# Optimization experiments

Measured on AMD Instinct MI355X. Metric: run time of the kernel, lower is better.

The kernel has to match this reference:

```python
import jax, jax.numpy as jnp
import numpy as np

DIM = 512
HIDDEN = 2048
BATCH = 16384
NUM_VECTORS = 3


def _mlp(z, W1, b1, W2, b2, W3, b3):
    # 3-layer tanh MLP: dim -> hidden -> hidden -> dim
    h = jnp.tanh(z @ W1.T + b1)
    h = jnp.tanh(h @ W2.T + b2)
    return h @ W3.T + b3


def setup_inputs() -> dict:
    key = jax.random.key(0)
    ks = jax.random.split(key, 10)
    t = jnp.zeros((1,), dtype=jnp.float32)
    augmented_state = jax.random.normal(ks[0], (BATCH, DIM + 1), dtype=jnp.float32)
    epsilons = jax.random.normal(ks[1], (NUM_VECTORS, BATCH, DIM), dtype=jnp.float32)
    # Xavier-normal-ish init with gain 0.1 (final layer randomized instead of the
    # original zero-init so outputs/grads are non-trivial for kernel testing).
    def xavier(k, fan_out, fan_in, gain=0.1):
        std = gain * np.sqrt(2.0 / (fan_in + fan_out))
        return (jax.random.normal(k, (fan_out, fan_in), dtype=jnp.float32) * std)
    W1 = xavier(ks[2], HIDDEN, DIM)
    b1 = jnp.zeros((HIDDEN,), dtype=jnp.float32)
    W2 = xavier(ks[3], HIDDEN, HIDDEN)
    b2 = jnp.zeros((HIDDEN,), dtype=jnp.float32)
    W3 = xavier(ks[4], DIM, HIDDEN)
    b3 = jnp.zeros((DIM,), dtype=jnp.float32)
    return {"t": t, "augmented_state": augmented_state, "epsilons": epsilons,
            "W1": W1, "b1": b1, "W2": W2, "b2": b2, "W3": W3, "b3": b3}


def reference(t, augmented_state, epsilons, W1, b1, W2, b2, W3, b3):
    dim = W1.shape[1]
    z = augmented_state[:, :dim]                      # [B, dim]
    dz_dt = _mlp(z, W1, b1, W2, b2, W3, b3)           # [B, dim]
    # torch code computes g = d(sum f(z))/dz = J^T @ 1 (same for every loop
    # iteration since only epsilon is resampled), then averages (g * eps).sum(1).
    g = jax.grad(lambda zz: _mlp(zz, W1, b1, W2, b2, W3, b3).sum())(z)  # [B, dim]
    num_vectors = epsilons.shape[0]
    trace = jnp.einsum('kbd,bd->b', epsilons, g)[:, None] / num_vectors  # [B, 1]
    return jnp.concatenate([dz_dt, trace], axis=1)    # [B, dim+1]
```

## Files before the change

### kernel.cpp

```cpp
#include <hip/hip_runtime.h>
#include <hip/hip_bf16.h>
#include <stdint.h>

#define DIM 512
#define HIDDEN 2048
#define BATCH 16384

using bf16 = __hip_bfloat16;
typedef float f32x4 __attribute__((ext_vector_type(4)));
typedef short bf16x8 __attribute__((ext_vector_type(8)));

__device__ __forceinline__ float bf2f(bf16 x) { return __bfloat162float(x); }
__device__ __forceinline__ bf16 f2bf(float x) { return __float2bfloat16(x); }

template <int MODE>
__global__ __launch_bounds__(256)
void gemm_bt(const bf16* __restrict__ A, const bf16* __restrict__ Bt,
             int M, int N, int K,
             const float* __restrict__ bias,
             float* __restrict__ outF,
             bf16* __restrict__ out1,
             bf16* __restrict__ out2,
             const float* __restrict__ u3,
             const bf16* __restrict__ h1s)
{
    __shared__ __align__(128) bf16 As[128 * 64];
    __shared__ __align__(128) bf16 Bs[128 * 64];

    const int tid  = threadIdx.x;
    const int lane = tid & 63;
    const int wave = tid >> 6;

    const int nwg = gridDim.x * gridDim.y;
    const int bid = blockIdx.y * gridDim.x + blockIdx.x;
    const int cpx = nwg >> 3;
    const int sw  = (bid & 7) * cpx + (bid >> 3);
    const int nbm = M >> 7;
    const int bm  = sw % nbm;
    const int bn  = sw / nbm;
    const int row0 = bm << 7;
    const int col0 = bn << 7;

    const int wr = wave >> 1;
    const int wc = wave & 1;

    f32x4 acc[4][4] = {};

    const int srow  = lane >> 3;
    const int sslot = lane & 7;

    const int KT = K >> 6;
    for (int kt = 0; kt < KT; ++kt) {
        const int k0 = kt << 6;
        __syncthreads();
#pragma unroll
        for (int i = 0; i < 4; ++i) {
            const int q   = wave * 4 + i;
            const int row = q * 8 + srow;
            const int gs  = sslot ^ (row & 7);
            const bf16* ga = A  + (size_t)(row0 + row) * K + (k0 + gs * 8);
            const bf16* gb = Bt + (size_t)(col0 + row) * K + (k0 + gs * 8);
            __builtin_amdgcn_global_load_lds(
                (const __attribute__((address_space(1))) void*)ga,
                (__attribute__((address_space(3))) void*)(As + q * 512), 16, 0, 0);
            __builtin_amdgcn_global_load_lds(
                (const __attribute__((address_space(1))) void*)gb,
                (__attribute__((address_space(3))) void*)(Bs + q * 512), 16, 0, 0);
        }
        __syncthreads();

#pragma unroll
        for (int half = 0; half < 2; ++half) {
            const int kb = half * 4 + (lane >> 4);
            bf16x8 af[4], bfr[4];
#pragma unroll
            for (int m = 0; m < 4; ++m) {
                const int ar = wr * 64 + m * 16 + (lane & 15);
                af[m] = *(const bf16x8*)((const char*)As + ar * 128 + ((kb ^ (ar & 7)) << 4));
            }
#pragma unroll
            for (int n = 0; n < 4; ++n) {
                const int br = wc * 64 + n * 16 + (lane & 15);
                bfr[n] = *(const bf16x8*)((const char*)Bs + br * 128 + ((kb ^ (br & 7)) << 4));
            }
#pragma unroll
            for (int m = 0; m < 4; ++m)
#pragma unroll
                for (int n = 0; n < 4; ++n)
                    acc[m][n] = __builtin_amdgcn_mfma_f32_16x16x32_bf16(
                        af[m], bfr[n], acc[m][n], 0, 0, 0);
        }
    }

    const int c_lo = lane & 15;
    const int c_hi = lane >> 4;
#pragma unroll
    for (int m = 0; m < 4; ++m) {
#pragma unroll
        for (int n = 0; n < 4; ++n) {
#pragma unroll
            for (int r = 0; r < 4; ++r) {
                const int grow = row0 + wr * 64 + m * 16 + c_hi * 4 + r;
                const int gcol = col0 + wc * 64 + n * 16 + c_lo;
                const float cv = acc[m][n][r];
                if (MODE == 0) {
                    float v = tanhf(cv + bias[gcol]);
                    out1[(size_t)grow * N + gcol] = f2bf(v);
                } else if (MODE == 1) {
                    float v = tanhf(cv + bias[gcol]);
                    out1[(size_t)grow * N + gcol] = f2bf(v);
                    out2[(size_t)grow * N + gcol] = f2bf(u3[gcol] * (1.0f - v * v));
                } else if (MODE == 2) {
                    outF[(size_t)grow * 513 + gcol] = cv + bias[gcol];
                } else if (MODE == 3) {
                    float h = bf2f(h1s[(size_t)grow * N + gcol]);
                    out1[(size_t)grow * N + gcol] = f2bf(cv * (1.0f - h * h));
                } else {
                    outF[(size_t)grow * N + gcol] = cv;
                }
            }
        }
    }
}


__global__ void eps_reduce(const float* __restrict__ eps, float* __restrict__ esum, int n)
{
    const float4* e0 = (const float4*)eps;
    const float4* e1 = (const float4*)(eps + (size_t)n);
    const float4* e2 = (const float4*)(eps + 2 * (size_t)n);
    float4* o = (float4*)esum;
    const int n4 = n >> 2;
    const int stride = gridDim.x * blockDim.x;
    for (int i = blockIdx.x * blockDim.x + threadIdx.x; i < n4; i += stride) {
        float4 a = e0[i], b = e1[i], c = e2[i];
        o[i] = make_float4(a.x + b.x + c.x, a.y + b.y + c.y,
                           a.z + b.z + c.z, a.w + b.w + c.w);
    }
}

__global__ void z_convert(const float* __restrict__ aug, bf16* __restrict__ zb)
{
    const int stride = gridDim.x * blockDim.x;
    for (int i = blockIdx.x * blockDim.x + threadIdx.x; i < BATCH * DIM; i += stride) {
        const int b = i >> 9, d = i & 511;
        zb[i] = f2bf(aug[(size_t)b * 513 + d]);
    }
}

__global__ void conv_bf16(const float* __restrict__ src, bf16* __restrict__ dst, int n)
{
    const int stride = gridDim.x * blockDim.x;
    for (int i = blockIdx.x * blockDim.x + threadIdx.x; i < n; i += stride)
        dst[i] = f2bf(src[i]);
}

__global__ void transpose_bf16(const float* __restrict__ src, bf16* __restrict__ dst,
                               int R, int C)
{
    __shared__ float t[32][33];
    const int bx = blockIdx.x * 32;
    const int by = blockIdx.y * 32;
    const int tx = threadIdx.x & 31;
    const int ty = threadIdx.x >> 5;
#pragma unroll
    for (int j = 0; j < 32; j += 8)
        t[ty + j][tx] = src[(size_t)(by + ty + j) * C + (bx + tx)];
    __syncthreads();
#pragma unroll
    for (int j = 0; j < 32; j += 8)
        dst[(size_t)(bx + ty + j) * R + (by + tx)] = f2bf(t[tx][ty + j]);
}

__global__ void colsum(const float* __restrict__ W3, float* __restrict__ u3)
{
    const int j = blockIdx.x * blockDim.x + threadIdx.x;
    if (j >= HIDDEN) return;
    float s = 0.f;
    for (int i = 0; i < DIM; ++i) s += W3[(size_t)i * HIDDEN + j];
    u3[j] = s;
}

__global__ void trace_kernel(const float* __restrict__ esum, const float* __restrict__ g,
                             float* __restrict__ out)
{
    const int row  = blockIdx.x * 4 + (threadIdx.x >> 6);
    const int lane = threadIdx.x & 63;
    const float4* e  = (const float4*)(esum + (size_t)row * 512);
    const float4* gg = (const float4*)(g + (size_t)row * 512);
    float s = 0.f;
#pragma unroll
    for (int i = 0; i < 2; ++i) {
        float4 a = e[lane * 2 + i], b = gg[lane * 2 + i];
        s += a.x * b.x + a.y * b.y + a.z * b.z + a.w * b.w;
    }
#pragma unroll
    for (int off = 1; off < 64; off <<= 1) s += __shfl_xor(s, off);
    if (lane == 0) out[(size_t)row * 513 + 512] = s * (1.0f / 3.0f);
}

extern "C" void kernel_launch(void* const* d_in, const int* in_sizes, int n_in,
                              void* d_out, int out_size, void* d_ws, size_t ws_size,
                              hipStream_t stream)
{
    const float* aug = (const float*)d_in[1];
    const float* eps = (const float*)d_in[2];
    const float* W1  = (const float*)d_in[3];
    const float* b1  = (const float*)d_in[4];
    const float* W2  = (const float*)d_in[5];
    const float* b2  = (const float*)d_in[6];
    const float* W3  = (const float*)d_in[7];
    const float* b3  = (const float*)d_in[8];
    float* out = (float*)d_out;

    char* ws = (char*)d_ws;
    size_t off = 0;
    auto alloc = [&](size_t bytes) {
        char* p = ws + off;
        off += (bytes + 255) & ~(size_t)255;
        return p;
    };
    bf16*  zb   = (bf16*)alloc((size_t)BATCH * DIM * 2);
    bf16*  h1   = (bf16*)alloc((size_t)BATCH * HIDDEN * 2);
    bf16*  h2   = (bf16*)alloc((size_t)BATCH * HIDDEN * 2);
    bf16*  d2   = (bf16*)alloc((size_t)BATCH * HIDDEN * 2);
    float* g    = (float*)alloc((size_t)BATCH * DIM * 4);
    float* esum = (float*)alloc((size_t)BATCH * DIM * 4);
    bf16*  W1b  = (bf16*)alloc((size_t)HIDDEN * DIM * 2);
    bf16*  W2b  = (bf16*)alloc((size_t)HIDDEN * HIDDEN * 2);
    bf16*  W3b  = (bf16*)alloc((size_t)DIM * HIDDEN * 2);
    bf16*  W2t  = (bf16*)alloc((size_t)HIDDEN * HIDDEN * 2);
    bf16*  W1t  = (bf16*)alloc((size_t)DIM * HIDDEN * 2);
    float* u3   = (float*)alloc((size_t)HIDDEN * 4);
    bf16*  d1   = h2;

    eps_reduce<<<2048, 256, 0, stream>>>(eps, esum, BATCH * DIM);
    z_convert<<<2048, 256, 0, stream>>>(aug, zb);
    conv_bf16<<<1024, 256, 0, stream>>>(W1, W1b, HIDDEN * DIM);
    conv_bf16<<<2048, 256, 0, stream>>>(W2, W2b, HIDDEN * HIDDEN);
    conv_bf16<<<1024, 256, 0, stream>>>(W3, W3b, DIM * HIDDEN);
    transpose_bf16<<<dim3(HIDDEN / 32, HIDDEN / 32), 256, 0, stream>>>(W2, W2t, HIDDEN, HIDDEN);
    transpose_bf16<<<dim3(DIM / 32, HIDDEN / 32), 256, 0, stream>>>(W1, W1t, HIDDEN, DIM);
    colsum<<<HIDDEN / 256, 256, 0, stream>>>(W3, u3);

    dim3 gBig(BATCH / 128, HIDDEN / 128);
    dim3 gSml(BATCH / 128, DIM / 128);
    gemm_bt<0><<<gBig, 256, 0, stream>>>(zb, W1b, BATCH, HIDDEN, DIM, b1,
                                         nullptr, h1, nullptr, nullptr, nullptr);
    gemm_bt<1><<<gBig, 256, 0, stream>>>(h1, W2b, BATCH, HIDDEN, HIDDEN, b2,
                                         nullptr, h2, d2, u3, nullptr);
    gemm_bt<2><<<gSml, 256, 0, stream>>>(h2, W3b, BATCH, DIM, HIDDEN, b3,
                                         out, nullptr, nullptr, nullptr, nullptr);
    gemm_bt<3><<<gBig, 256, 0, stream>>>(d2, W2t, BATCH, HIDDEN, HIDDEN, nullptr,
                                         nullptr, d1, nullptr, nullptr, h1);
    gemm_bt<4><<<gSml, 256, 0, stream>>>(d1, W1t, BATCH, DIM, HIDDEN, nullptr,
                                         g, nullptr, nullptr, nullptr, nullptr);
    trace_kernel<<<BATCH / 4, 256, 0, stream>>>(esum, g, out);
}
```

Baseline: 800.5 us.

## Add 256x256 double-buffered 8-wave GEMM with direct-to-LDS loads for big layers

Introduces a new gemm8 kernel with 256x256 tiles, 512 threads, and a 128KB double-buffered LDS ring. It stages tiles with global_load_lds and interleaves half-tile loads with MFMA phases under explicit barriers, waitcnts and setprio. The three large hidden-dimension GEMMs use it, and their tanh epilogues switch to an exp/rcp approximation. Block-index swizzling in the old kernel also changes from column-major to row-major ordering. The aim is more data reuse per tile and hiding of global-load latency, at the cost of lower occupancy and a slightly less accurate tanh.

```diff
diff --git a/kernel.cpp b/kernel.cpp
--- a/kernel.cpp
+++ b/kernel.cpp
@@ -12,17 +12,188 @@
 
 __device__ __forceinline__ float bf2f(bf16 x) { return __bfloat162float(x); }
 __device__ __forceinline__ bf16 f2bf(float x) { return __float2bfloat16(x); }
+
+__device__ __forceinline__ float fast_tanh(float x) {
+    float e = __expf(2.0f * x);
+    return 1.0f - 2.0f * __builtin_amdgcn_rcpf(e + 1.0f);
+}
+
+__device__ __forceinline__ f32x4 mfma16(bf16x8 a, bf16x8 b, f32x4 c) {
+    return __builtin_amdgcn_mfma_f32_16x16x32_bf16(a, b, c, 0, 0, 0);
+}
+
+__device__ __forceinline__ void BARP() {
+    __builtin_amdgcn_sched_barrier(0);
+    __builtin_amdgcn_s_barrier();
+    __builtin_amdgcn_sched_barrier(0);
+}
+__device__ __forceinline__ void LGK0_SB() {
+    asm volatile("s_waitcnt lgkmcnt(0)" ::: "memory");
+    __builtin_amdgcn_sched_barrier(0);
+}
+__device__ __forceinline__ void VMC4() {
+    asm volatile("s_waitcnt vmcnt(4)" ::: "memory");
+}
+
+__device__ __forceinline__ void stage_half(const bf16* __restrict__ G, int grow0,
+                                           int Kdim, int kbase, bf16* lds,
+                                           int elem_base, int wave, int srow4, int gs8)
+{
+#pragma unroll
+    for (int i = 0; i < 2; ++i) {
+        const int q = wave * 2 + i;
+        const bf16* ga = G + (size_t)(grow0 + q * 16 + srow4) * Kdim + kbase + gs8;
+        __builtin_amdgcn_global_load_lds(
+            (const __attribute__((address_space(1))) void*)ga,
+            (__attribute__((address_space(3))) void*)(lds + elem_base + q * 512), 16, 0, 0);
+    }
+}
+
+template <int MODE>
+__global__ __launch_bounds__(512, 2)
+void gemm8(const bf16* __restrict__ A, const bf16* __restrict__ Bt,
+           int M, int N, int K,
+           const float* __restrict__ bias,
+           bf16* __restrict__ out1, bf16* __restrict__ out2,
+           const float* __restrict__ u3, const bf16* __restrict__ h1s)
+{
+    __shared__ bf16 lds[65536];
+    const int tid  = threadIdx.x;
+    const int lane = tid & 63;
+    const int wave = tid >> 6;
+
+    const int nwg = gridDim.x * gridDim.y;
+    const int bid = blockIdx.y * gridDim.x + blockIdx.x;
+    const int cpx = nwg >> 3;
+    const int sw  = (bid & 7) * cpx + (bid >> 3);
+    const int nbn = N >> 8;
+    const int bm  = sw / nbn;
+    const int bn  = sw % nbn;
+    const int row0 = bm << 8;
+    const int col0 = bn << 8;
+
+    const int wr = wave >> 2;
+    const int wc = wave & 3;
+    const int l15 = lane & 15;
+
+    const int slotl    = (((lane >> 4) ^ (l15 & 3)) << 4);
+    const int laneoffA = (wr * 128 + l15) * 64 + slotl;
+    const int laneoffB = (wc * 64  + l15) * 64 + slotl;
+    const int srow4 = lane >> 2;
+    const int gs8   = (((lane & 3) ^ ((lane >> 2) & 3)) << 3);
+
+    const char* ldsc = (const char*)lds;
+    f32x4 acc[8][4] = {};
+    bf16x8 af[8];
+
+    stage_half(A,  row0, K, 0,  lds, 0,     wave, srow4, gs8);
+    stage_half(Bt, col0, K, 0,  lds, 16384, wave, srow4, gs8);
+    stage_half(A,  row0, K, 32, lds, 8192,  wave, srow4, gs8);
+    stage_half(Bt, col0, K, 32, lds, 24576, wave, srow4, gs8);
+    VMC4(); BARP();
+
+    const int KT = K >> 6;
+    for (int t = 0; t < KT; ++t) {
+        const int cur = t & 1;
+        const int cb  = cur << 16;
+        const int ce  = (cur ^ 1) << 15;
+        const int knt = ((t + 1 < KT) ? t + 1 : 0) << 6;
+
+#pragma unroll
+        for (int m = 0; m < 8; ++m)
+            af[m] = *(const bf16x8*)(ldsc + cb + m * 1024 + laneoffA);
+        bf16x8 b0 = *(const bf16x8*)(ldsc + cb + 32768 + laneoffB);
+        bf16x8 b1 = *(const bf16x8*)(ldsc + cb + 32768 + 1024 + laneoffB);
+        stage_half(A, row0, K, knt, lds, ce, wave, srow4, gs8);
+        BARP(); LGK0_SB();
+        __builtin_amdgcn_s_setprio(1);
+#pragma unroll
+        for (int m = 0; m < 8; ++m) {
+            acc[m][0] = mfma16(af[m], b0, acc[m][0]);
+            acc[m][1] = mfma16(af[m], b1, acc[m][1]);
+        }
+        __builtin_amdgcn_s_setprio(0);
+        BARP();
+
+        b0 = *(const bf16x8*)(ldsc + cb + 32768 + 2048 + laneoffB);
+        b1 = *(const bf16x8*)(ldsc + cb + 32768 + 3072 + laneoffB);
+        stage_half(Bt, col0, K, knt, lds, ce + 16384, wave, srow4, gs8);
+        BARP(); LGK0_SB();
+        __builtin_amdgcn_s_setprio(1);
+#pragma unroll
+        for (int m = 0; m < 8; ++m) {
+            acc[m][2] = mfma16(af[m], b0, acc[m][2]);
+            acc[m][3] = mfma16(af[m], b1, acc[m][3]);
+        }
+        __builtin_amdgcn_s_setprio(0);
+        VMC4();
+        BARP();
+
+#pragma unroll
+        for (int m = 0; m < 8; ++m)
+            af[m] = *(const bf16x8*)(ldsc + cb + 16384 + m * 1024 + laneoffA);
+        b0 = *(const bf16x8*)(ldsc + cb + 49152 + laneoffB);
+        b1 = *(const bf16x8*)(ldsc + cb + 49152 + 1024 + laneoffB);
+        stage_half(A, row0, K, knt + 32, lds, ce + 8192, wave, srow4, gs8);
+        BARP(); LGK0_SB();
+        __builtin_amdgcn_s_setprio(1);
+#pragma unroll
+        for (int m = 0; m < 8; ++m) {
+            acc[m][0] = mfma16(af[m], b0, acc[m][0]);
+            acc[m][1] = mfma16(af[m], b1, acc[m][1]);
+        }
+        __builtin_amdgcn_s_setprio(0);
+        BARP();
+
+        b0 = *(const bf16x8*)(ldsc + cb + 49152 + 2048 + laneoffB);
+        b1 = *(const bf16x8*)(ldsc + cb + 49152 + 3072 + laneoffB);
+        stage_half(Bt, col0, K, knt + 32, lds, ce + 24576, wave, srow4, gs8);
+        BARP(); LGK0_SB();
+        __builtin_amdgcn_s_setprio(1);
+#pragma unroll
+        for (int m = 0; m < 8; ++m) {
+            acc[m][2] = mfma16(af[m], b0, acc[m][2]);
+            acc[m][3] = mfma16(af[m], b1, acc[m][3]);
+        }
+        __builtin_amdgcn_s_setprio(0);
+        VMC4();
+        BARP();
+    }
+
+    const int c4 = (lane >> 4) << 2;
+#pragma unroll
+    for (int m = 0; m < 8; ++m) {
+        const int growb = row0 + wr * 128 + m * 16 + c4;
+#pragma unroll
+        for (int n = 0; n < 4; ++n) {
+            const int gcol = col0 + wc * 64 + n * 16 + l15;
+            const float bz = (MODE == 3) ? 0.0f : bias[gcol];
+            const float uu = (MODE == 1) ? u3[gcol] : 0.0f;
+#pragma unroll
+            for (int r = 0; r < 4; ++r) {
+                const size_t idx = (size_t)(growb + r) * N + gcol;
+                const float cv = acc[m][n][r];
+                if (MODE == 0) {
+                    out1[idx] = f2bf(fast_tanh(cv + bz));
+                } else if (MODE == 1) {
+                    float v = fast_tanh(cv + bz);
+                    out1[idx] = f2bf(v);
+                    out2[idx] = f2bf(uu * (1.0f - v * v));
+                } else {
+                    float h = bf2f(h1s[idx]);
+                    out1[idx] = f2bf(cv * (1.0f - h * h));
+                }
+            }
+        }
+    }
+}
 
 template <int MODE>
 __global__ __launch_bounds__(256)
 void gemm_bt(const bf16* __restrict__ A, const bf16* __restrict__ Bt,
              int M, int N, int K,
              const float* __restrict__ bias,
-             float* __restrict__ outF,
-             bf16* __restrict__ out1,
-             bf16* __restrict__ out2,
-             const float* __restrict__ u3,
-             const bf16* __restrict__ h1s)
+             float* __restrict__ outF)
 {
     __shared__ __align__(128) bf16 As[128 * 64];
     __shared__ __align__(128) bf16 Bs[128 * 64];
@@ -35,9 +206,9 @@
     const int bid = blockIdx.y * gridDim.x + blockIdx.x;
     const int cpx = nwg >> 3;
     const int sw  = (bid & 7) * cpx + (bid >> 3);
-    const int nbm = M >> 7;
-    const int bm  = sw % nbm;
-    const int bn  = sw / nbm;
+    const int nbn = N >> 7;
+    const int bm  = sw / nbn;
+    const int bn  = sw % nbn;
     const int row0 = bm << 7;
     const int col0 = bn << 7;
 
@@ -87,8 +258,7 @@
             for (int m = 0; m < 4; ++m)
 #pragma unroll
                 for (int n = 0; n < 4; ++n)
-                    acc[m][n] = __builtin_amdgcn_mfma_f32_16x16x32_bf16(
-                        af[m], bfr[n], acc[m][n], 0, 0, 0);
+                    acc[m][n] = mfma16(af[m], bfr[n], acc[m][n]);
         }
     }
 
@@ -103,18 +273,8 @@
                 const int grow = row0 + wr * 64 + m * 16 + c_hi * 4 + r;
                 const int gcol = col0 + wc * 64 + n * 16 + c_lo;
                 const float cv = acc[m][n][r];
-                if (MODE == 0) {
-                    float v = tanhf(cv + bias[gcol]);
-                    out1[(size_t)grow * N + gcol] = f2bf(v);
-                } else if (MODE == 1) {
-                    float v = tanhf(cv + bias[gcol]);
-                    out1[(size_t)grow * N + gcol] = f2bf(v);
-                    out2[(size_t)grow * N + gcol] = f2bf(u3[gcol] * (1.0f - v * v));
-                } else if (MODE == 2) {
+                if (MODE == 2) {
                     outF[(size_t)grow * 513 + gcol] = cv + bias[gcol];
-                } else if (MODE == 3) {
-                    float h = bf2f(h1s[(size_t)grow * N + gcol]);
-                    out1[(size_t)grow * N + gcol] = f2bf(cv * (1.0f - h * h));
                 } else {
                     outF[(size_t)grow * N + gcol] = cv;
                 }
@@ -243,17 +403,15 @@
     transpose_bf16<<<dim3(DIM / 32, HIDDEN / 32), 256, 0, stream>>>(W1, W1t, HIDDEN, DIM);
     colsum<<<HIDDEN / 256, 256, 0, stream>>>(W3, u3);
 
-    dim3 gBig(BATCH / 128, HIDDEN / 128);
+    dim3 g8(BATCH / 256, HIDDEN / 256);
     dim3 gSml(BATCH / 128, DIM / 128);
-    gemm_bt<0><<<gBig, 256, 0, stream>>>(zb, W1b, BATCH, HIDDEN, DIM, b1,
-                                         nullptr, h1, nullptr, nullptr, nullptr);
-    gemm_bt<1><<<gBig, 256, 0, stream>>>(h1, W2b, BATCH, HIDDEN, HIDDEN, b2,
-                                         nullptr, h2, d2, u3, nullptr);
-    gemm_bt<2><<<gSml, 256, 0, stream>>>(h2, W3b, BATCH, DIM, HIDDEN, b3,
-                                         out, nullptr, nullptr, nullptr, nullptr);
-    gemm_bt<3><<<gBig, 256, 0, stream>>>(d2, W2t, BATCH, HIDDEN, HIDDEN, nullptr,
-                                         nullptr, d1, nullptr, nullptr, h1);
-    gemm_bt<4><<<gSml, 256, 0, stream>>>(d1, W1t, BATCH, DIM, HIDDEN, nullptr,
-                                         g, nullptr, nullptr, nullptr, nullptr);
+    gemm8<0><<<g8, 512, 0, stream>>>(zb, W1b, BATCH, HIDDEN, DIM, b1,
+                                     h1, nullptr, nullptr, nullptr);
+    gemm8<1><<<g8, 512, 0, stream>>>(h1, W2b, BATCH, HIDDEN, HIDDEN, b2,
+                                     h2, d2, u3, nullptr);
+    gemm_bt<2><<<gSml, 256, 0, stream>>>(h2, W3b, BATCH, DIM, HIDDEN, b3, out);
+    gemm8<3><<<g8, 512, 0, stream>>>(d2, W2t, BATCH, HIDDEN, HIDDEN, nullptr,
+                                     d1, nullptr, nullptr, h1);
+    gemm_bt<4><<<gSml, 256, 0, stream>>>(d1, W1t, BATCH, DIM, HIDDEN, nullptr, g);
     trace_kernel<<<BATCH / 4, 256, 0, stream>>>(esum, g, out);
 }
```

After: 687.5 us. -14.1%, faster.
